# Kernel tuning notes

Measured on AMD Instinct MI355X. Metric: run time of the kernel, lower is better.

Reference implementation:

```python
import jax, jax.numpy as jnp
import numpy as np

B=4; L=1024; NF=64; DM=256; DS=16; SCS=8; NL=4; DI=512; DTR=16; DC=4; NFM=6; NH=4; SCALES=(5,20,50)

def _ln(x,g,b):
    m=x.mean(-1,keepdims=True); v=((x-m)**2).mean(-1,keepdims=True)
    return (x-m)*jax.lax.rsqrt(v+1e-5)*g+b

def _scan(dA,dBu,C):
    # sequential selective scan: h_t = dA_t*h + dBu_t ; y_t = sum_n h_t * C_t
    def step(h,inp):
        a,bu,c=inp
        h=a*h+bu
        return h, jnp.einsum('bdn,bn->bd',h,c)
    h0=jnp.zeros(dA.shape[:1]+dA.shape[2:],dA.dtype)
    _,ys=jax.lax.scan(step,h0,(dA.swapaxes(0,1),dBu.swapaxes(0,1),C.swapaxes(0,1)))
    return ys.swapaxes(0,1)  # [B,L,DI]

def _mamba(x,g,b,inw,cw,cb,xpw,dtw,dtb,Alog,Dp,outw,ds):
    # MambaBlock: LN -> SelectiveSSM -> residual (dropout=identity in eval)
    xn=_ln(x,g,b)
    u,z=jnp.split(xn@inw.T,2,-1)
    k=cw.T[:,None,:]  # torch depthwise Conv1d weight [DI,1,DC] -> WIO [DC,1,DI]
    u=jax.lax.conv_general_dilated(u,k,(1,),[(cw.shape[1]-1,0)],dimension_numbers=('NWC','WIO','NWC'),feature_group_count=u.shape[-1])+cb
    u=jax.nn.silu(u)
    A=-jnp.exp(Alog)                     # [DI,ds]
    xd=u@xpw.T                           # [B,L,DTR+2*ds]
    dt=jax.nn.softplus(xd[...,:DTR]@dtw.T+dtb)   # [B,L,DI]
    Bm=xd[...,DTR:DTR+ds]; Cm=xd[...,DTR+ds:]
    dA=jnp.exp(dt[...,None]*A)                   # [B,L,DI,ds]
    dBu=dt[...,None]*Bm[:,:,None,:]*u[...,None]  # [B,L,DI,ds]
    y=_scan(dA,dBu,Cm)+u*Dp
    return x+(y*jax.nn.silu(z))@outw.T

def _mha(x,wqkv,bqkv,wout,bout):
    Bq,S,E=x.shape; hd=E//NH
    q,k,v=jnp.split(x@wqkv.T+bqkv,3,-1)
    sp=lambda t: t.reshape(Bq,S,NH,hd).transpose(0,2,1,3)
    att=jax.nn.softmax(jnp.einsum('bhqd,bhkd->bhqk',sp(q),sp(k))*(1.0/np.sqrt(hd)),-1)
    o=jnp.einsum('bhqk,bhkd->bhqd',att,sp(v)).transpose(0,2,1,3).reshape(Bq,S,E)
    return o@wout.T+bout

def _forward(x,in_w,in_b,in_ln_g,in_ln_b,mb_ln_g,mb_ln_b,mb_in_w,mb_conv_w,mb_conv_b,mb_xp_w,mb_dt_w,mb_dt_b,mb_Alog,mb_D,mb_out_w,sc_ln_g,sc_ln_b,sc_in_w,sc_conv_w,sc_conv_b,sc_xp_w,sc_dt_w,sc_dt_b,sc_Alog,sc_D,sc_out_w,fus_qkv_w,fus_qkv_b,fus_out_w,fus_out_b,ms_out_w,ms_out_b,sa_ln1_g,sa_ln1_b,sa_ln2_g,sa_ln2_b,sa_qkv_w,sa_qkv_b,sa_out_w,sa_out_b,sa_ff1_w,sa_ff1_b,sa_ff2_w,sa_ff2_b,ev1_w,ev1_b,ev2_w,ev2_b,ttf1_w,ttf1_b,ttf2_w,ttf2_b,emb_w,emb_b):
    gelu=lambda t: jax.nn.gelu(t,approximate=False)
    h=gelu(_ln(x@in_w.T+in_b,in_ln_g,in_ln_b))
    for i in range(NL):
        h=_mamba(h,mb_ln_g[i],mb_ln_b[i],mb_in_w[i],mb_conv_w[i],mb_conv_b[i],mb_xp_w[i],mb_dt_w[i],mb_dt_b[i],mb_Alog[i],mb_D[i],mb_out_w[i],DS)
    pooled=[]
    for i,s in enumerate(SCALES):
        p=_mamba(h[:,-s:,:],sc_ln_g[i],sc_ln_b[i],sc_in_w[i],sc_conv_w[i],sc_conv_b[i],sc_xp_w[i],sc_dt_w[i],sc_dt_b[i],sc_Alog[i],sc_D[i],sc_out_w[i],SCS)
        pooled.append(p.mean(1))  # AdaptiveAvgPool1d(1)
    stack=jnp.stack(pooled,1)  # [B,3,DM]
    fused=_mha(stack,fus_qkv_w,fus_qkv_b,fus_out_w,fus_out_b).reshape(x.shape[0],-1)@ms_out_w.T+ms_out_b
    s2=stack+_mha(_ln(stack,sa_ln1_g,sa_ln1_b),sa_qkv_w,sa_qkv_b,sa_out_w,sa_out_b)
    att=s2+(gelu(_ln(s2,sa_ln2_g,sa_ln2_b)@sa_ff1_w.T+sa_ff1_b)@sa_ff2_w.T+sa_ff2_b)
    final=fused+att.mean(1)
    ev=jax.nn.softplus(gelu(final@ev1_w.T+ev1_b)@ev2_w.T+ev2_b)
    alpha=ev+1.0
    Ssum=alpha.sum(-1,keepdims=True)
    probs=alpha/Ssum; unc=(NFM+1)/Ssum
    ttf=gelu(final@ttf1_w.T+ttf1_b)@ttf2_w.T+ttf2_b
    tm=jax.nn.softplus(ttf[:,:NFM]); ts=jnp.exp(0.5*ttf[:,NFM:])
    emb=final@emb_w.T+emb_b
    # concat of (probs, evidence, alpha, uncertainty, ttf_mean, ttf_std, embedding) -> [B,162]
    return jnp.concatenate([probs,ev,alpha,unc,tm,ts,emb],-1)

def setup_inputs():
    ks=iter(jax.random.split(jax.random.key(0),64))
    nk=lambda: next(ks)
    w=lambda *s: jax.random.normal(nk(),s,jnp.float32)*0.02
    z=lambda *s: jnp.zeros(s,jnp.float32)
    o=lambda *s: jnp.ones(s,jnp.float32)
    Al=lambda n,ds: jnp.broadcast_to(jnp.log(jnp.arange(1,ds+1,dtype=jnp.float32)),(n,DI,ds))
    return dict(x=jax.random.normal(nk(),(B,L,NF),jnp.float32),
        in_w=w(DM,NF), in_b=z(DM), in_ln_g=o(DM), in_ln_b=z(DM),
        mb_ln_g=o(NL,DM), mb_ln_b=z(NL,DM), mb_in_w=w(NL,2*DI,DM), mb_conv_w=w(NL,DI,DC), mb_conv_b=z(NL,DI),
        mb_xp_w=w(NL,DTR+2*DS,DI), mb_dt_w=w(NL,DI,DTR), mb_dt_b=z(NL,DI), mb_Alog=Al(NL,DS), mb_D=o(NL,DI), mb_out_w=w(NL,DM,DI),
        sc_ln_g=o(3,DM), sc_ln_b=z(3,DM), sc_in_w=w(3,2*DI,DM), sc_conv_w=w(3,DI,DC), sc_conv_b=z(3,DI),
        sc_xp_w=w(3,DTR+2*SCS,DI), sc_dt_w=w(3,DI,DTR), sc_dt_b=z(3,DI), sc_Alog=Al(3,SCS), sc_D=o(3,DI), sc_out_w=w(3,DM,DI),
        fus_qkv_w=w(3*DM,DM), fus_qkv_b=z(3*DM), fus_out_w=w(DM,DM), fus_out_b=z(DM), ms_out_w=w(DM,3*DM), ms_out_b=z(DM),
        sa_ln1_g=o(DM), sa_ln1_b=z(DM), sa_ln2_g=o(DM), sa_ln2_b=z(DM),
        sa_qkv_w=w(3*DM,DM), sa_qkv_b=z(3*DM), sa_out_w=w(DM,DM), sa_out_b=z(DM),
        sa_ff1_w=w(4*DM,DM), sa_ff1_b=z(4*DM), sa_ff2_w=w(DM,4*DM), sa_ff2_b=z(DM),
        ev1_w=w(DM,DM), ev1_b=z(DM), ev2_w=w(NFM+1,DM), ev2_b=z(NFM+1),
        ttf1_w=w(DM//2,DM), ttf1_b=z(DM//2), ttf2_w=w(2*NFM,DM//2), ttf2_b=z(2*NFM),
        emb_w=w(DM//2,DM), emb_b=z(DM//2))

def reference(x,in_w,in_b,in_ln_g,in_ln_b,mb_ln_g,mb_ln_b,mb_in_w,mb_conv_w,mb_conv_b,mb_xp_w,mb_dt_w,mb_dt_b,mb_Alog,mb_D,mb_out_w,sc_ln_g,sc_ln_b,sc_in_w,sc_conv_w,sc_conv_b,sc_xp_w,sc_dt_w,sc_dt_b,sc_Alog,sc_D,sc_out_w,fus_qkv_w,fus_qkv_b,fus_out_w,fus_out_b,ms_out_w,ms_out_b,sa_ln1_g,sa_ln1_b,sa_ln2_g,sa_ln2_b,sa_qkv_w,sa_qkv_b,sa_out_w,sa_out_b,sa_ff1_w,sa_ff1_b,sa_ff2_w,sa_ff2_b,ev1_w,ev1_b,ev2_w,ev2_b,ttf1_w,ttf1_b,ttf2_w,ttf2_b,emb_w,emb_b):
    return _forward(x,in_w,in_b,in_ln_g,in_ln_b,mb_ln_g,mb_ln_b,mb_in_w,mb_conv_w,mb_conv_b,mb_xp_w,mb_dt_w,mb_dt_b,mb_Alog,mb_D,mb_out_w,sc_ln_g,sc_ln_b,sc_in_w,sc_conv_w,sc_conv_b,sc_xp_w,sc_dt_w,sc_dt_b,sc_Alog,sc_D,sc_out_w,fus_qkv_w,fus_qkv_b,fus_out_w,fus_out_b,ms_out_w,ms_out_b,sa_ln1_g,sa_ln1_b,sa_ln2_g,sa_ln2_b,sa_qkv_w,sa_qkv_b,sa_out_w,sa_out_b,sa_ff1_w,sa_ff1_b,sa_ff2_w,sa_ff2_b,ev1_w,ev1_b,ev2_w,ev2_b,ttf1_w,ttf1_b,ttf2_w,ttf2_b,emb_w,emb_b)
```

## Files before the change

kernel.cpp:

```cpp
#include <hip/hip_runtime.h>
#include <math.h>


typedef short short8v __attribute__((ext_vector_type(8)));
typedef float f32x4   __attribute__((ext_vector_type(4)));

__device__ __forceinline__ float geluf(float x){ return 0.5f*x*(1.0f + erff(x*0.70710678118654752f)); }
__device__ __forceinline__ float softplusf_(float x){ return (x > 20.f) ? x : log1pf(expf(x)); }
__device__ __forceinline__ unsigned short f2bf(float f){
  unsigned int u = __float_as_uint(f);
  unsigned int r = (u + 0x7FFFu + ((u >> 16) & 1u)) >> 16;
  return (unsigned short)r;
}

__device__ __forceinline__ void sc_region(int r, int& z, int& roff, int& s){
  if (r < 64){ z=0; roff=0; s=5; }
  else if (r < 192){ z=1; roff=64; s=20; }
  else { z=2; roff=192; s=50; }
}

__global__ __launch_bounds__(256) void k_f2b_all(
    const float* s0, unsigned short* d0,
    const float* s1, unsigned short* d1,
    const float* s2, unsigned short* d2,
    const float* s3, unsigned short* d3,
    const float* s4, unsigned short* d4,
    const float* s5, unsigned short* d5)
{
  int blk = blockIdx.x;
  const float* s; unsigned short* d; int base;
  if      (blk < 1024){ s=s0; d=d0; base=0; }
  else if (blk < 1536){ s=s1; d=d1; base=1024; }
  else if (blk < 1632){ s=s2; d=d2; base=1536; }
  else if (blk < 2400){ s=s3; d=d3; base=1632; }
  else if (blk < 2784){ s=s4; d=d4; base=2400; }
  else                { s=s5; d=d5; base=2784; }
  int i = ((blk - base)*256 + threadIdx.x)*4;
  float4 v = *(const float4*)(s + i);
  *(ushort4*)(d + i) = make_ushort4(f2bf(v.x), f2bf(v.y), f2bf(v.z), f2bf(v.w));
}

__global__ __launch_bounds__(256) void k_inproj(
    const float* __restrict__ x, const float* __restrict__ w,
    const float* __restrict__ b, const float* __restrict__ g,
    const float* __restrict__ beta, float* __restrict__ h)
{
  __shared__ float xr[64];
  __shared__ float r1[4], r2[4];
  int row = blockIdx.x;
  int tid = threadIdx.x;
  if (tid < 64) xr[tid] = x[row*64 + tid];
  __syncthreads();
  float acc = b[tid];
  const float* wr = w + tid*64;
  #pragma unroll
  for (int k = 0; k < 64; k++) acc += xr[k]*wr[k];
  float s1 = acc, s2 = acc*acc;
  #pragma unroll
  for (int o = 32; o > 0; o >>= 1){ s1 += __shfl_down(s1,o,64); s2 += __shfl_down(s2,o,64); }
  if ((tid & 63) == 0){ r1[tid>>6] = s1; r2[tid>>6] = s2; }
  __syncthreads();
  float S1 = r1[0]+r1[1]+r1[2]+r1[3];
  float S2 = r2[0]+r2[1]+r2[2]+r2[3];
  float m = S1*(1.f/256.f);
  float var = S2*(1.f/256.f) - m*m;
  float xn = (acc - m)*rsqrtf(var + 1e-5f)*g[tid] + beta[tid];
  h[row*256 + tid] = geluf(xn);
}

__global__ __launch_bounds__(256) void k_ln(
    const float* __restrict__ src, const float* __restrict__ g, const float* __restrict__ beta,
    unsigned short* __restrict__ dst)
{
  __shared__ float r1[4], r2[4];
  int r = blockIdx.x, tid = threadIdx.x;
  float v = src[r*256 + tid];
  float s1 = v, s2 = v*v;
  #pragma unroll
  for (int o = 32; o > 0; o >>= 1){ s1 += __shfl_down(s1,o,64); s2 += __shfl_down(s2,o,64); }
  if ((tid & 63) == 0){ r1[tid>>6] = s1; r2[tid>>6] = s2; }
  __syncthreads();
  float S1 = r1[0]+r1[1]+r1[2]+r1[3];
  float S2 = r2[0]+r2[1]+r2[2]+r2[3];
  float m = S1*(1.f/256.f);
  float var = S2*(1.f/256.f) - m*m;
  dst[r*256 + tid] = f2bf((v - m)*rsqrtf(var + 1e-5f)*g[tid] + beta[tid]);
}

__global__ __launch_bounds__(256) void k_ln_sc(
    const float* __restrict__ h, const float* __restrict__ gb, const float* __restrict__ bb,
    unsigned short* __restrict__ dst, float* __restrict__ stack)
{
  __shared__ float r1[4], r2[4];
  int r = blockIdx.x, tid = threadIdx.x;
  if (r >= 448){
    int idx = (r - 448)*256 + tid;
    if (idx < 3072) stack[idx] = 0.f;
    return;
  }
  int z, roff, s; sc_region(r, z, roff, s);
  int local = r - roff;
  if (local >= 4*s) return;
  int b = local / s, t = local % s;
  float v = h[(b*1024 + (1024 - s) + t)*256 + tid];
  const float* g = gb + z*256; const float* be = bb + z*256;
  float s1 = v, s2 = v*v;
  #pragma unroll
  for (int o = 32; o > 0; o >>= 1){ s1 += __shfl_down(s1,o,64); s2 += __shfl_down(s2,o,64); }
  if ((tid & 63) == 0){ r1[tid>>6] = s1; r2[tid>>6] = s2; }
  __syncthreads();
  float S1 = r1[0]+r1[1]+r1[2]+r1[3];
  float S2 = r2[0]+r2[1]+r2[2]+r2[3];
  float m = S1*(1.f/256.f);
  float var = S2*(1.f/256.f) - m*m;
  dst[r*256 + tid] = f2bf((v - m)*rsqrtf(var + 1e-5f)*g[tid] + be[tid]);
}

template<int MODE, int SCB>
__global__ __launch_bounds__(256) void k_mm64(
    const unsigned short* __restrict__ A, const unsigned short* __restrict__ Wb,
    float* __restrict__ C,
    const float* __restrict__ resid,
    float* __restrict__ pool_out,
    int M, int N, int K, int wstr)
{
  int tid = threadIdx.x;
  int wave = tid >> 6, lane = tid & 63;
  int mh = wave & 1, nh = wave >> 1;
  int m0 = blockIdx.y*64 + mh*32;
  int n0 = blockIdx.x*64 + nh*32;
  int z = 0, roff = 0, sc = 0;
  const unsigned short* W = Wb;
  if (SCB){ sc_region(blockIdx.y*64, z, roff, sc); W += z*wstr; }
  int lrow = lane & 15, kc = lane >> 4;
  f32x4 acc[2][2] = {{{0.f,0.f,0.f,0.f},{0.f,0.f,0.f,0.f}},{{0.f,0.f,0.f,0.f},{0.f,0.f,0.f,0.f}}};
  for (int k0 = 0; k0 < K; k0 += 32){
    short8v a[2], b[2];
    #pragma unroll
    for (int mi = 0; mi < 2; mi++){
      int r = m0 + mi*16 + lrow; r = min(r, M-1);
      a[mi] = *(const short8v*)(A + r*K + k0 + kc*8);
    }
    #pragma unroll
    for (int ni = 0; ni < 2; ni++){
      int c = n0 + ni*16 + lrow;
      b[ni] = *(const short8v*)(W + c*K + k0 + kc*8);
    }
    #pragma unroll
    for (int mi = 0; mi < 2; mi++)
      #pragma unroll
      for (int ni = 0; ni < 2; ni++)
        acc[mi][ni] = __builtin_amdgcn_mfma_f32_16x16x32_bf16(a[mi], b[ni], acc[mi][ni], 0, 0, 0);
  }
  int rb = kc*4;
  #pragma unroll
  for (int mi = 0; mi < 2; mi++){
    #pragma unroll
    for (int rr = 0; rr < 4; rr++){
      int grow = m0 + mi*16 + rb + rr;
      if (grow >= M) continue;
      #pragma unroll
      for (int ni = 0; ni < 2; ni++){
        int gcol = n0 + ni*16 + lrow;
        float v = acc[mi][ni][rr];
        if (MODE == 0){
          C[grow*N + gcol] = v;
        } else if (MODE == 1){
          C[grow*N + gcol] = resid[grow*256 + gcol] + v;
        } else {
          int local = grow - roff;
          if (local < 4*sc){
            int bb2 = local / sc, t = local % sc;
            float rv = resid[(bb2*1024 + (1024 - sc) + t)*256 + gcol] + v;
            atomicAdd(&pool_out[bb2*768 + z*256 + gcol], rv*(1.f/(float)sc));
          }
        }
      }
    }
  }
}

__global__ __launch_bounds__(256) void k_conv(
    const float* __restrict__ uz, const float* __restrict__ cw, const float* __restrict__ cb,
    float* __restrict__ uc, unsigned short* __restrict__ ucb)
{
  int row = blockIdx.x;
  int t = row & 1023;
  int tid = threadIdx.x;
  for (int d = tid; d < 512; d += 256){
    float acc = cb[d];
    const float* w = cw + d*4;
    #pragma unroll
    for (int k = 0; k < 4; k++){
      int ts = t - 3 + k;
      if (ts >= 0) acc += uz[(long)(row - (3-k))*1024 + d]*w[k];
    }
    float s = acc/(1.f + expf(-acc));
    uc[(long)row*512 + d] = s;
    ucb[(long)row*512 + d] = f2bf(s);
  }
}

__global__ __launch_bounds__(256) void k_conv_sc(
    const float* __restrict__ uz, const float* __restrict__ cwb, const float* __restrict__ cbb,
    float* __restrict__ uc, unsigned short* __restrict__ ucb)
{
  int row = blockIdx.x;
  int z, roff, s; sc_region(row, z, roff, s);
  int local = row - roff;
  if (local >= 4*s) return;
  int t = local % s;
  const float* cw = cwb + z*2048;
  const float* cb = cbb + z*512;
  int tid = threadIdx.x;
  for (int d = tid; d < 512; d += 256){
    float acc = cb[d];
    const float* w = cw + d*4;
    #pragma unroll
    for (int k = 0; k < 4; k++){
      int ts = t - 3 + k;
      if (ts >= 0) acc += uz[(long)(row - (3-k))*1024 + d]*w[k];
    }
    float sv = acc/(1.f + expf(-acc));
    uc[(long)row*512 + d] = sv;
    ucb[(long)row*512 + d] = f2bf(sv);
  }
}

template<int NT, int SCB>
__global__ __launch_bounds__(512) void k_xpdt(
    const unsigned short* __restrict__ A, const unsigned short* __restrict__ Wb,
    float* __restrict__ xdout,
    const float* __restrict__ dtwb, const float* __restrict__ dtbb,
    float* __restrict__ dtout, int M)
{
  const int K = 512;
  const int NC = NT*16;
  __shared__ float pacc[8][16][NC];
  __shared__ float sxd[16][16];
  int tid = threadIdx.x;
  int wave = tid >> 6, lane = tid & 63;
  int bm0 = blockIdx.x*16;
  const unsigned short* W = Wb;
  const float* dtw = dtwb;
  const float* dtb = dtbb;
  if (SCB){
    int z, roff, s; sc_region(bm0, z, roff, s);
    W += z*(NC*K); dtw += z*8192; dtb += z*512;
  }
  int lrow = lane & 15, kc = lane >> 4;
  int kbase = wave*64;
  f32x4 acc[NT];
  #pragma unroll
  for (int ni = 0; ni < NT; ni++) acc[ni] = (f32x4){0.f,0.f,0.f,0.f};
  #pragma unroll
  for (int k0 = 0; k0 < 64; k0 += 32){
    short8v a = *(const short8v*)(A + (long)(bm0 + lrow)*K + kbase + k0 + kc*8);
    #pragma unroll
    for (int ni = 0; ni < NT; ni++){
      short8v b = *(const short8v*)(W + (ni*16 + lrow)*K + kbase + k0 + kc*8);
      acc[ni] = __builtin_amdgcn_mfma_f32_16x16x32_bf16(a, b, acc[ni], 0, 0, 0);
    }
  }
  int rb = kc*4;
  #pragma unroll
  for (int rr = 0; rr < 4; rr++)
    #pragma unroll
    for (int ni = 0; ni < NT; ni++)
      pacc[wave][rb + rr][ni*16 + lrow] = acc[ni][rr];
  __syncthreads();
  for (int e = tid; e < 16*NC; e += 512){
    int r = e / NC, c = e % NC;
    float v = pacc[0][r][c] + pacc[1][r][c] + pacc[2][r][c] + pacc[3][r][c]
            + pacc[4][r][c] + pacc[5][r][c] + pacc[6][r][c] + pacc[7][r][c];
    xdout[(bm0 + r)*NC + c] = v;
    if (c < 16) sxd[r][c] = v;
  }
  __syncthreads();
  int d0 = tid;
  float w0[16];
  #pragma unroll
  for (int j = 0; j < 16; j++) w0[j] = dtw[d0*16 + j];
  float b0 = dtb[d0];
  #pragma unroll
  for (int r = 0; r < 16; r++){
    float a0 = b0;
    #pragma unroll
    for (int j = 0; j < 16; j++)
      a0 = fmaf(sxd[r][j], w0[j], a0);
    dtout[(bm0 + r)*512 + d0] = softplusf_(a0);
  }
}

__global__ __launch_bounds__(256) void k_scan_p1y(
    const float* __restrict__ dt, const float* __restrict__ uc,
    const float* __restrict__ xd, const float* __restrict__ Alog,
    float* __restrict__ hend, float* __restrict__ sdtb,
    float* __restrict__ yloc, float* __restrict__ Scum)
{
  const int CL = 64, NCH = 16;
  __shared__ float sdt[64][64], suc[64][64];
  __shared__ float sBC[64][32];
  int tid = threadIdx.x;
  int dblk = blockIdx.x;
  int b = blockIdx.y, ch = blockIdx.z;
  int t0 = ch*CL;
  for (int e = tid; e < CL*16; e += 256){
    int t = e >> 4, q = (e & 15)*4;
    long off = (long)(b*1024 + t0 + t)*512 + dblk*64 + q;
    *(float4*)&sdt[t][q] = *(const float4*)(dt + off);
    *(float4*)&suc[t][q] = *(const float4*)(uc + off);
  }
  for (int e = tid; e < CL*8; e += 256){
    int t = e >> 3, q = (e & 7)*4;
    *(float4*)&sBC[t][q] = *(const float4*)(xd + (long)(b*1024 + t0 + t)*48 + 16 + q);
  }
  __syncthreads();
  if (tid < 64){
    int d = dblk*64 + tid;
    float A[16];
    #pragma unroll
    for (int n = 0; n < 16; n++) A[n] = -__expf(Alog[d*16 + n]);
    float h[16];
    #pragma unroll
    for (int n = 0; n < 16; n++) h[n] = 0.f;
    float Ss = 0.f;
    #pragma unroll 2
    for (int t = 0; t < CL; t++){
      float dtv = sdt[t][tid];
      float uv  = suc[t][tid];
      Ss += dtv;
      float du = dtv*uv;
      float y = 0.f;
      #pragma unroll
      for (int n = 0; n < 16; n++){
        h[n] = fmaf(__expf(dtv*A[n]), h[n], du*sBC[t][n]);
        y = fmaf(h[n], sBC[t][16+n], y);
      }
      long row = (long)(b*1024 + t0 + t);
      yloc[row*512 + d] = y;
      Scum[row*512 + d] = Ss;
    }
    int base = ((b*NCH + ch)*512 + d)*16;
    #pragma unroll
    for (int q = 0; q < 4; q++)
      *(float4*)(hend + base + q*4) = make_float4(h[q*4], h[q*4+1], h[q*4+2], h[q*4+3]);
    sdtb[(b*NCH + ch)*512 + d] = Ss;
  }
}

__global__ __launch_bounds__(256) void k_scomb(
    const float* __restrict__ hend, const float* __restrict__ sdtb,
    const float* __restrict__ Alog, float* __restrict__ hstart,
    float* __restrict__ Aneg)
{
  const int NCH = 16;
  int idx = blockIdx.x*256 + threadIdx.x;
  int low = idx & 8191;
  int d = (idx >> 4) & 511, b = idx >> 13;
  float A = -__expf(Alog[low]);
  if (b == 0) Aneg[low] = A;
  float hs = 0.f;
  hstart[(b*NCH)*8192 + low] = 0.f;
  for (int c = 0; c < NCH-1; c++){
    float S  = sdtb[(b*NCH + c)*512 + d];
    float he = hend[(b*NCH + c)*8192 + low];
    hs = fmaf(__expf(A*S), hs, he);
    hstart[(b*NCH + c + 1)*8192 + low] = hs;
  }
}

__global__ __launch_bounds__(256) void k_corr(
    const float* __restrict__ yloc, const float* __restrict__ Scum,
    const float* __restrict__ hstart, const float* __restrict__ Aneg,
    const float* __restrict__ xd, const float* __restrict__ uc,
    const float* __restrict__ uz, const float* __restrict__ Dp,
    unsigned short* __restrict__ yg)
{
  __shared__ float sC[16];
  int row = blockIdx.x, tid = threadIdx.x;
  int b = row >> 10, t = row & 1023, ch = t >> 6;
  if (tid < 16) sC[tid] = xd[row*48 + 32 + tid];
  __syncthreads();
  #pragma unroll
  for (int rep = 0; rep < 2; rep++){
    int d = tid + rep*256;
    float Ss = Scum[row*512 + d];
    float y  = yloc[row*512 + d];
    const float* hs = hstart + ((b*16 + ch)*512 + d)*16;
    const float* An = Aneg + d*16;
    #pragma unroll
    for (int n = 0; n < 16; n++)
      y = fmaf(__expf(An[n]*Ss)*hs[n], sC[n], y);
    float uv = uc[row*512 + d];
    y = fmaf(uv, Dp[d], y);
    float zv = uz[(long)row*1024 + 512 + d];
    yg[row*512 + d] = f2bf(y*(zv/(1.f + __expf(-zv))));
  }
}

__global__ __launch_bounds__(64) void k_scan_sc(
    const float* __restrict__ dt, const float* __restrict__ uc,
    const float* __restrict__ uz, const float* __restrict__ xd,
    const float* __restrict__ Alogb, const float* __restrict__ Dpb,
    unsigned short* __restrict__ yg)
{
  __shared__ float sdt[52][64], suc[52][64], sz[52][64];
  __shared__ float sBC[52][16];
  int tid = threadIdx.x;
  int dblk = blockIdx.x;
  int d = dblk*64 + tid;
  int b = blockIdx.y, z = blockIdx.z;
  int s = (z==0) ? 5 : (z==1) ? 20 : 50;
  int roff = (z==0) ? 0 : (z==1) ? 64 : 192;
  const float* Alog = Alogb + z*4096;
  const float* Dp   = Dpb + z*512;
  float A[8];
  #pragma unroll
  for (int n = 0; n < 8; n++) A[n] = -__expf(Alog[d*8 + n]);
  float Dv = Dp[d];
  for (int e = tid; e < s*16; e += 64){
    int t = e >> 4, q = (e & 15)*4;
    long row = (long)(roff + b*s + t);
    *(float4*)&sdt[t][q] = *(const float4*)(dt + row*512 + dblk*64 + q);
    *(float4*)&suc[t][q] = *(const float4*)(uc + row*512 + dblk*64 + q);
    *(float4*)&sz[t][q]  = *(const float4*)(uz + row*1024 + 512 + dblk*64 + q);
  }
  for (int e = tid; e < s*4; e += 64){
    int t = e >> 2, q = (e & 3)*4;
    long row = (long)(roff + b*s + t);
    *(float4*)&sBC[t][q] = *(const float4*)(xd + row*32 + 16 + q);
  }
  __syncthreads();
  float h[8];
  #pragma unroll
  for (int n = 0; n < 8; n++) h[n] = 0.f;
  for (int t = 0; t < s; t++){
    float dtv = sdt[t][tid];
    float uv  = suc[t][tid];
    float zv  = sz[t][tid];
    float du = dtv*uv;
    float y = 0.f;
    #pragma unroll
    for (int n = 0; n < 8; n++){
      h[n] = fmaf(__expf(dtv*A[n]), h[n], du*sBC[t][n]);
      y = fmaf(h[n], sBC[t][8+n], y);
    }
    y = fmaf(uv, Dv, y);
    float gate = zv/(1.f + __expf(-zv));
    yg[(long)(roff + b*s + t)*512 + d] = f2bf(y*gate);
  }
}

template<int M, int ACT, int RES>
__global__ __launch_bounds__(256) void k_tw(
    const float* __restrict__ A, const float* __restrict__ W,
    const float* __restrict__ bias, float* __restrict__ out,
    const float* __restrict__ resid, int N, int K, int ostride, int ocoff)
{
  extern __shared__ float sx[];
  int tid = threadIdx.x;
  for (int e = tid*4; e < M*K; e += 1024)
    *(float4*)&sx[e] = *(const float4*)(A + e);
  __syncthreads();
  int wave = tid >> 6, lane = tid & 63;
  int c = blockIdx.x*4 + wave;
  if (c >= N) return;
  float acc[M];
  #pragma unroll
  for (int r = 0; r < M; r++) acc[r] = 0.f;
  for (int k = lane*4; k < K; k += 256){
    float4 w4 = *(const float4*)(W + c*K + k);
    #pragma unroll
    for (int r = 0; r < M; r++){
      float4 x4 = *(float4*)&sx[r*K + k];
      acc[r] = fmaf(x4.x,w4.x,fmaf(x4.y,w4.y,fmaf(x4.z,w4.z,fmaf(x4.w,w4.w,acc[r]))));
    }
  }
  #pragma unroll
  for (int r = 0; r < M; r++){
    #pragma unroll
    for (int o = 32; o > 0; o >>= 1) acc[r] += __shfl_down(acc[r], o, 64);
  }
  if (lane == 0){
    float bv = bias[c];
    #pragma unroll
    for (int r = 0; r < M; r++){
      float v = acc[r] + bv;
      if (ACT == 1) v = geluf(v);
      if (RES == 1) v += resid[r*256 + c];
      out[r*ostride + ocoff + c] = v;
    }
  }
}

__global__ __launch_bounds__(256) void k_t_ln(
    const float* __restrict__ src, const float* __restrict__ g, const float* __restrict__ b,
    float* __restrict__ dst)
{
  __shared__ float r1[4], r2[4];
  int r = blockIdx.x, tid = threadIdx.x;
  float v = src[r*256 + tid];
  float s1 = v, s2 = v*v;
  #pragma unroll
  for (int o = 32; o > 0; o >>= 1){ s1 += __shfl_down(s1,o,64); s2 += __shfl_down(s2,o,64); }
  if ((tid & 63) == 0){ r1[tid>>6] = s1; r2[tid>>6] = s2; }
  __syncthreads();
  float S1 = r1[0]+r1[1]+r1[2]+r1[3];
  float S2 = r2[0]+r2[1]+r2[2]+r2[3];
  float m = S1*(1.f/256.f);
  float var = S2*(1.f/256.f) - m*m;
  dst[r*256 + tid] = (v - m)*rsqrtf(var + 1e-5f)*g[tid] + b[tid];
}

__global__ __launch_bounds__(256) void k_t_att(
    const float* __restrict__ qkv, float* __restrict__ ov)
{
  __shared__ float att[36];
  int b = blockIdx.x, tid = threadIdx.x;
  if (tid < 36){
    int hh = tid/9, r = (tid%9)/3, c = tid%3;
    float s = 0.f;
    const float* qp = qkv + (b*3 + r)*768 + hh*64;
    const float* kp = qkv + (b*3 + c)*768 + 256 + hh*64;
    for (int k = 0; k < 64; k++) s += qp[k]*kp[k];
    att[hh*9 + r*3 + c] = s*0.125f;
  }
  __syncthreads();
  if (tid < 12){
    int hh = tid/3, r = tid%3;
    float a0 = att[hh*9+r*3+0], a1 = att[hh*9+r*3+1], a2 = att[hh*9+r*3+2];
    float m = fmaxf(a0, fmaxf(a1, a2));
    float e0 = expf(a0-m), e1 = expf(a1-m), e2 = expf(a2-m);
    float s = e0+e1+e2;
    att[hh*9+r*3+0] = e0/s; att[hh*9+r*3+1] = e1/s; att[hh*9+r*3+2] = e2/s;
  }
  __syncthreads();
  for (int e = tid; e < 768; e += 256){
    int p = e >> 8, i = e & 255, hh = i >> 6;
    ov[(b*3 + p)*256 + i] = att[hh*9+p*3+0]*qkv[(b*3+0)*768+512+i]
                          + att[hh*9+p*3+1]*qkv[(b*3+1)*768+512+i]
                          + att[hh*9+p*3+2]*qkv[(b*3+2)*768+512+i];
  }
}

__global__ __launch_bounds__(256) void k_t_final(
    const float* __restrict__ fusedv, const float* __restrict__ s2f, float* __restrict__ finalv)
{
  int b = blockIdx.x, c = threadIdx.x;
  finalv[b*256 + c] = fusedv[b*256 + c] +
    (s2f[(b*3+0)*256 + c] + s2f[(b*3+1)*256 + c] + s2f[(b*3+2)*256 + c])*(1.f/3.f);
}

__global__ __launch_bounds__(64) void k_t_fin(
    const float* __restrict__ evraw, const float* __restrict__ ttraw, float* __restrict__ out)
{
  __shared__ float ev[7];
  __shared__ float S;
  int b = blockIdx.x, tid = threadIdx.x;
  if (tid < 7) ev[tid] = softplusf_(evraw[b*7 + tid]);
  __syncthreads();
  if (tid == 0){
    float s = 0.f;
    for (int j = 0; j < 7; j++) s += ev[j] + 1.f;
    S = s;
  }
  __syncthreads();
  float* ob = out + b*162;
  if (tid < 7){
    float al = ev[tid] + 1.f;
    ob[tid] = al / S;
    ob[7 + tid] = ev[tid];
    ob[14 + tid] = al;
  }
  if (tid == 0) ob[21] = 7.f / S;
  if (tid < 6){
    ob[22 + tid] = softplusf_(ttraw[b*12 + tid]);
    ob[28 + tid] = expf(0.5f*ttraw[b*12 + 6 + tid]);
  }
}

extern "C" void kernel_launch(void* const* d_in, const int* in_sizes, int n_in,
                              void* d_out, int out_size, void* d_ws, size_t ws_size,
                              hipStream_t stream)
{
  const float* x         = (const float*)d_in[0];
  const float* in_w      = (const float*)d_in[1];
  const float* in_b      = (const float*)d_in[2];
  const float* in_ln_g   = (const float*)d_in[3];
  const float* in_ln_b   = (const float*)d_in[4];
  const float* mb_ln_g   = (const float*)d_in[5];
  const float* mb_ln_b   = (const float*)d_in[6];
  const float* mb_in_w   = (const float*)d_in[7];
  const float* mb_conv_w = (const float*)d_in[8];
  const float* mb_conv_b = (const float*)d_in[9];
  const float* mb_xp_w   = (const float*)d_in[10];
  const float* mb_dt_w   = (const float*)d_in[11];
  const float* mb_dt_b   = (const float*)d_in[12];
  const float* mb_Alog   = (const float*)d_in[13];
  const float* mb_D      = (const float*)d_in[14];
  const float* mb_out_w  = (const float*)d_in[15];
  const float* sc_ln_g   = (const float*)d_in[16];
  const float* sc_ln_b   = (const float*)d_in[17];
  const float* sc_in_w   = (const float*)d_in[18];
  const float* sc_conv_w = (const float*)d_in[19];
  const float* sc_conv_b = (const float*)d_in[20];
  const float* sc_xp_w   = (const float*)d_in[21];
  const float* sc_dt_w   = (const float*)d_in[22];
  const float* sc_dt_b   = (const float*)d_in[23];
  const float* sc_Alog   = (const float*)d_in[24];
  const float* sc_D      = (const float*)d_in[25];
  const float* sc_out_w  = (const float*)d_in[26];
  const float* fus_qkv_w = (const float*)d_in[27];
  const float* fus_qkv_b = (const float*)d_in[28];
  const float* fus_out_w = (const float*)d_in[29];
  const float* fus_out_b = (const float*)d_in[30];
  const float* ms_out_w  = (const float*)d_in[31];
  const float* ms_out_b  = (const float*)d_in[32];
  const float* sa_ln1_g  = (const float*)d_in[33];
  const float* sa_ln1_b  = (const float*)d_in[34];
  const float* sa_ln2_g  = (const float*)d_in[35];
  const float* sa_ln2_b  = (const float*)d_in[36];
  const float* sa_qkv_w  = (const float*)d_in[37];
  const float* sa_qkv_b  = (const float*)d_in[38];
  const float* sa_out_w  = (const float*)d_in[39];
  const float* sa_out_b  = (const float*)d_in[40];
  const float* sa_ff1_w  = (const float*)d_in[41];
  const float* sa_ff1_b  = (const float*)d_in[42];
  const float* sa_ff2_w  = (const float*)d_in[43];
  const float* sa_ff2_b  = (const float*)d_in[44];
  const float* ev1_w     = (const float*)d_in[45];
  const float* ev1_b     = (const float*)d_in[46];
  const float* ev2_w     = (const float*)d_in[47];
  const float* ev2_b     = (const float*)d_in[48];
  const float* ttf1_w    = (const float*)d_in[49];
  const float* ttf1_b    = (const float*)d_in[50];
  const float* ttf2_w    = (const float*)d_in[51];
  const float* ttf2_b    = (const float*)d_in[52];
  const float* emb_w     = (const float*)d_in[53];
  const float* emb_b     = (const float*)d_in[54];

  float* ws = (float*)d_ws;
  float* h     = ws;
  float* uz    = h    + 1048576;
  float* uc    = uz   + 4194304;
  float* dtb_  = uc   + 2097152;
  float* xd    = dtb_ + 2097152;
  float* stack = xd   + 196608;
  float* hend   = stack + 4096;
  float* hstart = hend + 524288;
  float* sdtb   = hstart + 524288;
  float* yloc   = sdtb + 32768;
  float* Scum   = yloc + 2097152;
  float* Aneg   = Scum + 2097152;
  float* qkvF   = Aneg + 8192;
  float* ovF    = qkvF + 9216;
  float* moF    = ovF  + 3072;
  float* fusedv = moF  + 3072;
  float* lnbuf  = fusedv + 1024;
  float* qkvS   = lnbuf + 3072;
  float* ovS    = qkvS + 9216;
  float* s2     = ovS  + 3072;
  float* ln2r   = s2   + 3072;
  float* hid    = ln2r + 3072;
  float* s2f    = hid  + 12288;
  float* finalv = s2f  + 3072;
  float* evh    = finalv + 1024;
  float* tth    = evh  + 1024;
  float* evraw  = tth  + 512;
  float* ttraw  = evraw + 32;
  float* fp32_end = ttraw + 64;
  unsigned short* bfb = (unsigned short*)fp32_end;
  unsigned short* xnb    = bfb;
  unsigned short* ucb    = xnb + 1048576;
  unsigned short* ygb    = ucb + 2097152;
  unsigned short* wmbin  = ygb + 2097152;
  unsigned short* wmbout = wmbin + 1048576;
  unsigned short* wmbxp  = wmbout + 524288;
  unsigned short* wscin  = wmbxp + 98304;
  unsigned short* wscout = wscin + 786432;
  unsigned short* wscxp  = wscout + 393216;

  k_f2b_all<<<2832, 256, 0, stream>>>(mb_in_w, wmbin, mb_out_w, wmbout, mb_xp_w, wmbxp,
                                      sc_in_w, wscin, sc_out_w, wscout, sc_xp_w, wscxp);

  k_inproj<<<4096, 256, 0, stream>>>(x, in_w, in_b, in_ln_g, in_ln_b, h);

  for (int l = 0; l < 4; l++){
    const float* Al = mb_Alog + l*8192;
    k_ln<<<4096, 256, 0, stream>>>(h, mb_ln_g + l*256, mb_ln_b + l*256, xnb);
    {
      dim3 g(16, 64);
      k_mm64<0,0><<<g, 256, 0, stream>>>(xnb, wmbin + l*262144, uz,
                                         nullptr, nullptr, 4096, 1024, 256, 0);
    }
    k_conv<<<4096, 256, 0, stream>>>(uz, mb_conv_w + l*2048, mb_conv_b + l*512, uc, ucb);
    k_xpdt<3,0><<<256, 512, 0, stream>>>(ucb, wmbxp + l*24576, xd,
                                         mb_dt_w + l*8192, mb_dt_b + l*512, dtb_, 4096);
    {
      dim3 g(8, 4, 16);
      k_scan_p1y<<<g, 256, 0, stream>>>(dtb_, uc, xd, Al, hend, sdtb, yloc, Scum);
      k_scomb<<<128, 256, 0, stream>>>(hend, sdtb, Al, hstart, Aneg);
      k_corr<<<4096, 256, 0, stream>>>(yloc, Scum, hstart, Aneg, xd, uc, uz,
                                       mb_D + l*512, ygb);
    }
    {
      dim3 g(4, 64);
      k_mm64<1,0><<<g, 256, 0, stream>>>(ygb, wmbout + l*131072, h,
                                         h, nullptr, 4096, 256, 512, 0);
    }
  }

  k_ln_sc<<<460, 256, 0, stream>>>(h, sc_ln_g, sc_ln_b, xnb, stack);
  {
    dim3 g(16, 7);
    k_mm64<0,1><<<g, 256, 0, stream>>>(xnb, wscin, uz, nullptr, nullptr,
                                       448, 1024, 256, 262144);
  }
  k_conv_sc<<<448, 256, 0, stream>>>(uz, sc_conv_w, sc_conv_b, uc, ucb);
  k_xpdt<2,1><<<28, 512, 0, stream>>>(ucb, wscxp, xd, sc_dt_w, sc_dt_b, dtb_, 448);
  {
    dim3 g(8, 4, 3);
    k_scan_sc<<<g, 64, 0, stream>>>(dtb_, uc, uz, xd, sc_Alog, sc_D, ygb);
  }
  {
    dim3 g(4, 7);
    k_mm64<2,1><<<g, 256, 0, stream>>>(ygb, wscout, nullptr, h, stack,
                                       448, 256, 512, 131072);
  }

  float* dout = (float*)d_out;
  k_tw<12,0,0><<<192, 256, 12*256*4, stream>>>(stack, fus_qkv_w, fus_qkv_b, qkvF, nullptr, 768, 256, 768, 0);
  k_t_att<<<4, 256, 0, stream>>>(qkvF, ovF);
  k_tw<12,0,0><<<64, 256, 12*256*4, stream>>>(ovF, fus_out_w, fus_out_b, moF, nullptr, 256, 256, 256, 0);
  k_tw<4,0,0><<<64, 256, 4*768*4, stream>>>(moF, ms_out_w, ms_out_b, fusedv, nullptr, 256, 768, 256, 0);
  k_t_ln<<<12, 256, 0, stream>>>(stack, sa_ln1_g, sa_ln1_b, lnbuf);
  k_tw<12,0,0><<<192, 256, 12*256*4, stream>>>(lnbuf, sa_qkv_w, sa_qkv_b, qkvS, nullptr, 768, 256, 768, 0);
  k_t_att<<<4, 256, 0, stream>>>(qkvS, ovS);
  k_tw<12,0,1><<<64, 256, 12*256*4, stream>>>(ovS, sa_out_w, sa_out_b, s2, stack, 256, 256, 256, 0);
  k_t_ln<<<12, 256, 0, stream>>>(s2, sa_ln2_g, sa_ln2_b, ln2r);
  k_tw<12,1,0><<<256, 256, 12*256*4, stream>>>(ln2r, sa_ff1_w, sa_ff1_b, hid, nullptr, 1024, 256, 1024, 0);
  k_tw<12,0,1><<<64, 256, 12*1024*4, stream>>>(hid, sa_ff2_w, sa_ff2_b, s2f, s2, 256, 1024, 256, 0);
  k_t_final<<<4, 256, 0, stream>>>(fusedv, s2f, finalv);
  k_tw<4,1,0><<<64, 256, 4*256*4, stream>>>(finalv, ev1_w, ev1_b, evh, nullptr, 256, 256, 256, 0);
  k_tw<4,0,0><<<2, 256, 4*256*4, stream>>>(evh, ev2_w, ev2_b, evraw, nullptr, 7, 256, 7, 0);
  k_tw<4,1,0><<<32, 256, 4*256*4, stream>>>(finalv, ttf1_w, ttf1_b, tth, nullptr, 128, 256, 128, 0);
  k_tw<4,0,0><<<3, 256, 4*128*4, stream>>>(tth, ttf2_w, ttf2_b, ttraw, nullptr, 12, 128, 12, 0);
  k_tw<4,0,0><<<32, 256, 4*256*4, stream>>>(finalv, emb_w, emb_b, dout, nullptr, 128, 256, 162, 34);
  k_t_fin<<<4, 64, 0, stream>>>(evraw, ttraw, dout);
}
```

Measured before the change: 624.1 us.

## Store gate and conv output as bf16 and batch small tail kernels

The in-projection GEMM now writes the u half as fp32 into a narrower buffer and the z gate half as bf16. The fp32 conv output is dropped, so the scan and correction kernels read bf16 u and z and convert them on load. Separately, the tail launches are merged: the two QKV projections, both attentions, both output projections and the three head projections each run as one combined kernel. This cuts memory traffic and launch count, at the cost of bf16 rounding on u and z inside the scan.

New measurement: 620.7 us. No clear change (-0.5%).

```diff
diff --git a/kernel.cpp b/kernel.cpp
--- a/kernel.cpp
+++ b/kernel.cpp
@@ -11,6 +11,9 @@
   unsigned int u = __float_as_uint(f);
   unsigned int r = (u + 0x7FFFu + ((u >> 16) & 1u)) >> 16;
   return (unsigned short)r;
+}
+__device__ __forceinline__ float bf2f(unsigned short u){
+  return __uint_as_float(((unsigned int)u) << 16);
 }
 
 __device__ __forceinline__ void sc_region(int r, int& z, int& roff, int& s){
@@ -122,6 +125,7 @@
     float* __restrict__ C,
     const float* __restrict__ resid,
     float* __restrict__ pool_out,
+    unsigned short* __restrict__ zgb,
     int M, int N, int K, int wstr)
 {
   int tid = threadIdx.x;
@@ -164,7 +168,8 @@
         int gcol = n0 + ni*16 + lrow;
         float v = acc[mi][ni][rr];
         if (MODE == 0){
-          C[grow*N + gcol] = v;
+          if (gcol < 512) C[(long)grow*512 + gcol] = v;
+          else zgb[(long)grow*512 + (gcol - 512)] = f2bf(v);
         } else if (MODE == 1){
           C[grow*N + gcol] = resid[grow*256 + gcol] + v;
         } else {
@@ -181,8 +186,8 @@
 }
 
 __global__ __launch_bounds__(256) void k_conv(
-    const float* __restrict__ uz, const float* __restrict__ cw, const float* __restrict__ cb,
-    float* __restrict__ uc, unsigned short* __restrict__ ucb)
+    const float* __restrict__ uu, const float* __restrict__ cw, const float* __restrict__ cb,
+    unsigned short* __restrict__ ucb)
 {
   int row = blockIdx.x;
   int t = row & 1023;
@@ -193,17 +198,16 @@
     #pragma unroll
     for (int k = 0; k < 4; k++){
       int ts = t - 3 + k;
-      if (ts >= 0) acc += uz[(long)(row - (3-k))*1024 + d]*w[k];
+      if (ts >= 0) acc += uu[(long)(row - (3-k))*512 + d]*w[k];
     }
     float s = acc/(1.f + expf(-acc));
-    uc[(long)row*512 + d] = s;
     ucb[(long)row*512 + d] = f2bf(s);
   }
 }
 
 __global__ __launch_bounds__(256) void k_conv_sc(
-    const float* __restrict__ uz, const float* __restrict__ cwb, const float* __restrict__ cbb,
-    float* __restrict__ uc, unsigned short* __restrict__ ucb)
+    const float* __restrict__ uu, const float* __restrict__ cwb, const float* __restrict__ cbb,
+    unsigned short* __restrict__ ucb)
 {
   int row = blockIdx.x;
   int z, roff, s; sc_region(row, z, roff, s);
@@ -219,10 +223,9 @@
     #pragma unroll
     for (int k = 0; k < 4; k++){
       int ts = t - 3 + k;
-      if (ts >= 0) acc += uz[(long)(row - (3-k))*1024 + d]*w[k];
+      if (ts >= 0) acc += uu[(long)(row - (3-k))*512 + d]*w[k];
     }
     float sv = acc/(1.f + expf(-acc));
-    uc[(long)row*512 + d] = sv;
     ucb[(long)row*512 + d] = f2bf(sv);
   }
 }
@@ -293,7 +296,7 @@
 }
 
 __global__ __launch_bounds__(256) void k_scan_p1y(
-    const float* __restrict__ dt, const float* __restrict__ uc,
+    const float* __restrict__ dt, const unsigned short* __restrict__ ucb,
     const float* __restrict__ xd, const float* __restrict__ Alog,
     float* __restrict__ hend, float* __restrict__ sdtb,
     float* __restrict__ yloc, float* __restrict__ Scum)
@@ -309,7 +312,13 @@
     int t = e >> 4, q = (e & 15)*4;
     long off = (long)(b*1024 + t0 + t)*512 + dblk*64 + q;
     *(float4*)&sdt[t][q] = *(const float4*)(dt + off);
-    *(float4*)&suc[t][q] = *(const float4*)(uc + off);
+  }
+  for (int e = tid; e < CL*8; e += 256){
+    int t = e >> 3, q = (e & 7)*8;
+    long off = (long)(b*1024 + t0 + t)*512 + dblk*64 + q;
+    short8v u8 = *(const short8v*)(ucb + off);
+    #pragma unroll
+    for (int j = 0; j < 8; j++) suc[t][q + j] = bf2f((unsigned short)u8[j]);
   }
   for (int e = tid; e < CL*8; e += 256){
     int t = e >> 3, q = (e & 7)*4;
@@ -373,8 +382,8 @@
 __global__ __launch_bounds__(256) void k_corr(
     const float* __restrict__ yloc, const float* __restrict__ Scum,
     const float* __restrict__ hstart, const float* __restrict__ Aneg,
-    const float* __restrict__ xd, const float* __restrict__ uc,
-    const float* __restrict__ uz, const float* __restrict__ Dp,
+    const float* __restrict__ xd, const unsigned short* __restrict__ ucb,
+    const unsigned short* __restrict__ zgb, const float* __restrict__ Dp,
     unsigned short* __restrict__ yg)
 {
   __shared__ float sC[16];
@@ -392,16 +401,16 @@
     #pragma unroll
     for (int n = 0; n < 16; n++)
       y = fmaf(__expf(An[n]*Ss)*hs[n], sC[n], y);
-    float uv = uc[row*512 + d];
+    float uv = bf2f(ucb[(long)row*512 + d]);
     y = fmaf(uv, Dp[d], y);
-    float zv = uz[(long)row*1024 + 512 + d];
+    float zv = bf2f(zgb[(long)row*512 + d]);
     yg[row*512 + d] = f2bf(y*(zv/(1.f + __expf(-zv))));
   }
 }
 
 __global__ __launch_bounds__(64) void k_scan_sc(
-    const float* __restrict__ dt, const float* __restrict__ uc,
-    const float* __restrict__ uz, const float* __restrict__ xd,
+    const float* __restrict__ dt, const unsigned short* __restrict__ ucb,
+    const unsigned short* __restrict__ zgb, const float* __restrict__ xd,
     const float* __restrict__ Alogb, const float* __restrict__ Dpb,
     unsigned short* __restrict__ yg)
 {
@@ -423,8 +432,17 @@
     int t = e >> 4, q = (e & 15)*4;
     long row = (long)(roff + b*s + t);
     *(float4*)&sdt[t][q] = *(const float4*)(dt + row*512 + dblk*64 + q);
-    *(float4*)&suc[t][q] = *(const float4*)(uc + row*512 + dblk*64 + q);
-    *(float4*)&sz[t][q]  = *(const float4*)(uz + row*1024 + 512 + dblk*64 + q);
+  }
+  for (int e = tid; e < s*8; e += 64){
+    int t = e >> 3, q = (e & 7)*8;
+    long row = (long)(roff + b*s + t);
+    short8v u8 = *(const short8v*)(ucb + row*512 + dblk*64 + q);
+    short8v z8 = *(const short8v*)(zgb + row*512 + dblk*64 + q);
+    #pragma unroll
+    for (int j = 0; j < 8; j++){
+      suc[t][q + j] = bf2f((unsigned short)u8[j]);
+      sz[t][q + j]  = bf2f((unsigned short)z8[j]);
+    }
   }
   for (int e = tid; e < s*4; e += 64){
     int t = e >> 2, q = (e & 3)*4;
@@ -494,30 +512,56 @@
   }
 }
 
-__global__ __launch_bounds__(256) void k_t_ln(
-    const float* __restrict__ src, const float* __restrict__ g, const float* __restrict__ b,
-    float* __restrict__ dst)
-{
-  __shared__ float r1[4], r2[4];
-  int r = blockIdx.x, tid = threadIdx.x;
-  float v = src[r*256 + tid];
-  float s1 = v, s2 = v*v;
-  #pragma unroll
-  for (int o = 32; o > 0; o >>= 1){ s1 += __shfl_down(s1,o,64); s2 += __shfl_down(s2,o,64); }
-  if ((tid & 63) == 0){ r1[tid>>6] = s1; r2[tid>>6] = s2; }
-  __syncthreads();
-  float S1 = r1[0]+r1[1]+r1[2]+r1[3];
-  float S2 = r2[0]+r2[1]+r2[2]+r2[3];
-  float m = S1*(1.f/256.f);
-  float var = S2*(1.f/256.f) - m*m;
-  dst[r*256 + tid] = (v - m)*rsqrtf(var + 1e-5f)*g[tid] + b[tid];
-}
-
-__global__ __launch_bounds__(256) void k_t_att(
-    const float* __restrict__ qkv, float* __restrict__ ov)
+__global__ __launch_bounds__(256) void k_qkv2(
+    const float* __restrict__ A0, const float* __restrict__ A1,
+    const float* __restrict__ W0, const float* __restrict__ B0,
+    const float* __restrict__ W1, const float* __restrict__ B1,
+    float* __restrict__ O0, float* __restrict__ O1)
+{
+  __shared__ float sx[3072];
+  int tid = threadIdx.x;
+  int sel = blockIdx.x >= 192;
+  const float* A = sel ? A1 : A0;
+  for (int e = tid*4; e < 3072; e += 1024)
+    *(float4*)&sx[e] = *(const float4*)(A + e);
+  __syncthreads();
+  int wave = tid >> 6, lane = tid & 63;
+  int c = (blockIdx.x - (sel ? 192 : 0))*4 + wave;
+  const float* W = sel ? W1 : W0;
+  const float* B = sel ? B1 : B0;
+  float* O = sel ? O1 : O0;
+  float acc[12];
+  #pragma unroll
+  for (int r = 0; r < 12; r++) acc[r] = 0.f;
+  {
+    int k = lane*4;
+    float4 w4 = *(const float4*)(W + c*256 + k);
+    #pragma unroll
+    for (int r = 0; r < 12; r++){
+      float4 x4 = *(float4*)&sx[r*256 + k];
+      acc[r] = fmaf(x4.x,w4.x,fmaf(x4.y,w4.y,fmaf(x4.z,w4.z,fmaf(x4.w,w4.w,acc[r]))));
+    }
+  }
+  #pragma unroll
+  for (int r = 0; r < 12; r++){
+    #pragma unroll
+    for (int o = 32; o > 0; o >>= 1) acc[r] += __shfl_down(acc[r], o, 64);
+  }
+  if (lane == 0){
+    float bv = B[c];
+    #pragma unroll
+    for (int r = 0; r < 12; r++) O[r*768 + c] = acc[r] + bv;
+  }
+}
+
+__global__ __launch_bounds__(256) void k_att2(
+    const float* __restrict__ qkvF, float* __restrict__ ovF,
+    const float* __restrict__ qkvS, float* __restrict__ ovS)
 {
   __shared__ float att[36];
-  int b = blockIdx.x, tid = threadIdx.x;
+  int sel = blockIdx.x >> 2, b = blockIdx.x & 3, tid = threadIdx.x;
+  const float* qkv = sel ? qkvS : qkvF;
+  float* ov = sel ? ovS : ovF;
   if (tid < 36){
     int hh = tid/9, r = (tid%9)/3, c = tid%3;
     float s = 0.f;
@@ -542,6 +586,116 @@
                           + att[hh*9+p*3+1]*qkv[(b*3+1)*768+512+i]
                           + att[hh*9+p*3+2]*qkv[(b*3+2)*768+512+i];
   }
+}
+
+__global__ __launch_bounds__(256) void k_out2(
+    const float* __restrict__ ovF, const float* __restrict__ ovS,
+    const float* __restrict__ fow, const float* __restrict__ fob,
+    const float* __restrict__ sow, const float* __restrict__ sob,
+    const float* __restrict__ stack, float* __restrict__ moF, float* __restrict__ s2)
+{
+  __shared__ float sx[3072];
+  int tid = threadIdx.x;
+  int sel = blockIdx.x >= 64;
+  const float* A = sel ? ovS : ovF;
+  for (int e = tid*4; e < 3072; e += 1024)
+    *(float4*)&sx[e] = *(const float4*)(A + e);
+  __syncthreads();
+  int wave = tid >> 6, lane = tid & 63;
+  int c = (blockIdx.x - (sel ? 64 : 0))*4 + wave;
+  const float* W = sel ? sow : fow;
+  const float* B = sel ? sob : fob;
+  float acc[12];
+  #pragma unroll
+  for (int r = 0; r < 12; r++) acc[r] = 0.f;
+  {
+    int k = lane*4;
+    float4 w4 = *(const float4*)(W + c*256 + k);
+    #pragma unroll
+    for (int r = 0; r < 12; r++){
+      float4 x4 = *(float4*)&sx[r*256 + k];
+      acc[r] = fmaf(x4.x,w4.x,fmaf(x4.y,w4.y,fmaf(x4.z,w4.z,fmaf(x4.w,w4.w,acc[r]))));
+    }
+  }
+  #pragma unroll
+  for (int r = 0; r < 12; r++){
+    #pragma unroll
+    for (int o = 32; o > 0; o >>= 1) acc[r] += __shfl_down(acc[r], o, 64);
+  }
+  if (lane == 0){
+    float bv = B[c];
+    #pragma unroll
+    for (int r = 0; r < 12; r++){
+      float v = acc[r] + bv;
+      if (sel) s2[r*256 + c] = v + stack[r*256 + c];
+      else     moF[r*256 + c] = v;
+    }
+  }
+}
+
+__global__ __launch_bounds__(256) void k_heads(
+    const float* __restrict__ finalv,
+    const float* __restrict__ e1w, const float* __restrict__ e1b, float* __restrict__ evh,
+    const float* __restrict__ t1w, const float* __restrict__ t1b, float* __restrict__ tth,
+    const float* __restrict__ ew, const float* __restrict__ eb, float* __restrict__ dout)
+{
+  __shared__ float sx[1024];
+  int tid = threadIdx.x;
+  if (tid < 256){
+    float4 v = *(const float4*)(finalv + tid*4);
+    *(float4*)&sx[tid*4] = v;
+  }
+  __syncthreads();
+  int wave = tid >> 6, lane = tid & 63;
+  int blk = blockIdx.x;
+  const float* W; const float* B; int c; int which;
+  if (blk < 64){ which = 0; c = blk*4 + wave; W = e1w; B = e1b; }
+  else if (blk < 96){ which = 1; c = (blk - 64)*4 + wave; W = t1w; B = t1b; }
+  else { which = 2; c = (blk - 96)*4 + wave; W = ew; B = eb; }
+  float acc[4] = {0.f,0.f,0.f,0.f};
+  {
+    int k = lane*4;
+    float4 w4 = *(const float4*)(W + c*256 + k);
+    #pragma unroll
+    for (int r = 0; r < 4; r++){
+      float4 x4 = *(float4*)&sx[r*256 + k];
+      acc[r] = fmaf(x4.x,w4.x,fmaf(x4.y,w4.y,fmaf(x4.z,w4.z,fmaf(x4.w,w4.w,acc[r]))));
+    }
+  }
+  #pragma unroll
+  for (int r = 0; r < 4; r++){
+    #pragma unroll
+    for (int o = 32; o > 0; o >>= 1) acc[r] += __shfl_down(acc[r], o, 64);
+  }
+  if (lane == 0){
+    float bv = B[c];
+    #pragma unroll
+    for (int r = 0; r < 4; r++){
+      float v = acc[r] + bv;
+      if (which == 0) evh[r*256 + c] = geluf(v);
+      else if (which == 1) tth[r*128 + c] = geluf(v);
+      else dout[r*162 + 34 + c] = v;
+    }
+  }
+}
+
+__global__ __launch_bounds__(256) void k_t_ln(
+    const float* __restrict__ src, const float* __restrict__ g, const float* __restrict__ b,
+    float* __restrict__ dst)
+{
+  __shared__ float r1[4], r2[4];
+  int r = blockIdx.x, tid = threadIdx.x;
+  float v = src[r*256 + tid];
+  float s1 = v, s2 = v*v;
+  #pragma unroll
+  for (int o = 32; o > 0; o >>= 1){ s1 += __shfl_down(s1,o,64); s2 += __shfl_down(s2,o,64); }
+  if ((tid & 63) == 0){ r1[tid>>6] = s1; r2[tid>>6] = s2; }
+  __syncthreads();
+  float S1 = r1[0]+r1[1]+r1[2]+r1[3];
+  float S2 = r2[0]+r2[1]+r2[2]+r2[3];
+  float m = S1*(1.f/256.f);
+  float var = S2*(1.f/256.f) - m*m;
+  dst[r*256 + tid] = (v - m)*rsqrtf(var + 1e-5f)*g[tid] + b[tid];
 }
 
 __global__ __launch_bounds__(256) void k_t_final(
@@ -642,9 +796,8 @@
 
   float* ws = (float*)d_ws;
   float* h     = ws;
-  float* uz    = h    + 1048576;
-  float* uc    = uz   + 4194304;
-  float* dtb_  = uc   + 2097152;
+  float* uu    = h    + 1048576;
+  float* dtb_  = uu   + 2097152;
   float* xd    = dtb_ + 2097152;
   float* stack = xd   + 196608;
   float* hend   = stack + 4096;
@@ -673,7 +826,8 @@
   unsigned short* bfb = (unsigned short*)fp32_end;
   unsigned short* xnb    = bfb;
   unsigned short* ucb    = xnb + 1048576;
-  unsigned short* ygb    = ucb + 2097152;
+  unsigned short* zgb    = ucb + 2097152;
+  unsigned short* ygb    = zgb + 2097152;
   unsigned short* wmbin  = ygb + 2097152;
   unsigned short* wmbout = wmbin + 1048576;
   unsigned short* wmbxp  = wmbout + 524288;
@@ -691,61 +845,59 @@
     k_ln<<<4096, 256, 0, stream>>>(h, mb_ln_g + l*256, mb_ln_b + l*256, xnb);
     {
       dim3 g(16, 64);
-      k_mm64<0,0><<<g, 256, 0, stream>>>(xnb, wmbin + l*262144, uz,
-                                         nullptr, nullptr, 4096, 1024, 256, 0);
-    }
-    k_conv<<<4096, 256, 0, stream>>>(uz, mb_conv_w + l*2048, mb_conv_b + l*512, uc, ucb);
+      k_mm64<0,0><<<g, 256, 0, stream>>>(xnb, wmbin + l*262144, uu,
+                                         nullptr, nullptr, zgb, 4096, 1024, 256, 0);
+    }
+    k_conv<<<4096, 256, 0, stream>>>(uu, mb_conv_w + l*2048, mb_conv_b + l*512, ucb);
     k_xpdt<3,0><<<256, 512, 0, stream>>>(ucb, wmbxp + l*24576, xd,
                                          mb_dt_w + l*8192, mb_dt_b + l*512, dtb_, 4096);
     {
       dim3 g(8, 4, 16);
-      k_scan_p1y<<<g, 256, 0, stream>>>(dtb_, uc, xd, Al, hend, sdtb, yloc, Scum);
+      k_scan_p1y<<<g, 256, 0, stream>>>(dtb_, ucb, xd, Al, hend, sdtb, yloc, Scum);
       k_scomb<<<128, 256, 0, stream>>>(hend, sdtb, Al, hstart, Aneg);
-      k_corr<<<4096, 256, 0, stream>>>(yloc, Scum, hstart, Aneg, xd, uc, uz,
+      k_corr<<<4096, 256, 0, stream>>>(yloc, Scum, hstart, Aneg, xd, ucb, zgb,
                                        mb_D + l*512, ygb);
     }
     {
       dim3 g(4, 64);
       k_mm64<1,0><<<g, 256, 0, stream>>>(ygb, wmbout + l*131072, h,
-                                         h, nullptr, 4096, 256, 512, 0);
+                                         h, nullptr, nullptr, 4096, 256, 512, 0);
     }
   }
 
   k_ln_sc<<<460, 256, 0, stream>>>(h, sc_ln_g, sc_ln_b, xnb, stack);
   {
     dim3 g(16, 7);
-    k_mm64<0,1><<<g, 256, 0, stream>>>(xnb, wscin, uz, nullptr, nullptr,
+    k_mm64<0,1><<<g, 256, 0, stream>>>(xnb, wscin, uu, nullptr, nullptr, zgb,
                                        448, 1024, 256, 262144);
   }
-  k_conv_sc<<<448, 256, 0, stream>>>(uz, sc_conv_w, sc_conv_b, uc, ucb);
+  k_conv_sc<<<448, 256, 0, stream>>>(uu, sc_conv_w, sc_conv_b, ucb);
   k_xpdt<2,1><<<28, 512, 0, stream>>>(ucb, wscxp, xd, sc_dt_w, sc_dt_b, dtb_, 448);
   {
     dim3 g(8, 4, 3);
-    k_scan_sc<<<g, 64, 0, stream>>>(dtb_, uc, uz, xd, sc_Alog, sc_D, ygb);
+    k_scan_sc<<<g, 64, 0, stream>>>(dtb_, ucb, zgb, xd, sc_Alog, sc_D, ygb);
   }
   {
     dim3 g(4, 7);
-    k_mm64<2,1><<<g, 256, 0, stream>>>(ygb, wscout, nullptr, h, stack,
+    k_mm64<2,1><<<g, 256, 0, stream>>>(ygb, wscout, nullptr, h, stack, nullptr,
                                        448, 256, 512, 131072);
   }
 
   float* dout = (float*)d_out;
-  k_tw<12,0,0><<<192, 256, 12*256*4, stream>>>(stack, fus_qkv_w, fus_qkv_b, qkvF, nullptr, 768, 256, 768, 0);
-  k_t_att<<<4, 256, 0, stream>>>(qkvF, ovF);
-  k_tw<12,0,0><<<64, 256, 12*256*4, stream>>>(ovF, fus_out_w, fus_out_b, moF, nullptr, 256, 256, 256, 0);
+  k_t_ln<<<12, 256, 0, stream>>>(stack, sa_ln1_g, sa_ln1_b, lnbuf);
+  k_qkv2<<<384, 256, 0, stream>>>(stack, lnbuf, fus_qkv_w, fus_qkv_b,
+                                  sa_qkv_w, sa_qkv_b, qkvF, qkvS);
+  k_att2<<<8, 256, 0, stream>>>(qkvF, ovF, qkvS, ovS);
+  k_out2<<<128, 256, 0, stream>>>(ovF, ovS, fus_out_w, fus_out_b,
+                                  sa_out_w, sa_out_b, stack, moF, s2);
   k_tw<4,0,0><<<64, 256, 4*768*4, stream>>>(moF, ms_out_w, ms_out_b, fusedv, nullptr, 256, 768, 256, 0);
-  k_t_ln<<<12, 256, 0, stream>>>(stack, sa_ln1_g, sa_ln1_b, lnbuf);
-  k_tw<12,0,0><<<192, 256, 12*256*4, stream>>>(lnbuf, sa_qkv_w, sa_qkv_b, qkvS, nullptr, 768, 256, 768, 0);
-  k_t_att<<<4, 256, 0, stream>>>(qkvS, ovS);
-  k_tw<12,0,1><<<64, 256, 12*256*4, stream>>>(ovS, sa_out_w, sa_out_b, s2, stack, 256, 256, 256, 0);
   k_t_ln<<<12, 256, 0, stream>>>(s2, sa_ln2_g, sa_ln2_b, ln2r);
   k_tw<12,1,0><<<256, 256, 12*256*4, stream>>>(ln2r, sa_ff1_w, sa_ff1_b, hid, nullptr, 1024, 256, 1024, 0);
   k_tw<12,0,1><<<64, 256, 12*1024*4, stream>>>(hid, sa_ff2_w, sa_ff2_b, s2f, s2, 256, 1024, 256, 0);
   k_t_final<<<4, 256, 0, stream>>>(fusedv, s2f, finalv);
-  k_tw<4,1,0><<<64, 256, 4*256*4, stream>>>(finalv, ev1_w, ev1_b, evh, nullptr, 256, 256, 256, 0);
+  k_heads<<<128, 256, 0, stream>>>(finalv, ev1_w, ev1_b, evh, ttf1_w, ttf1_b, tth,
+                                   emb_w, emb_b, dout);
   k_tw<4,0,0><<<2, 256, 4*256*4, stream>>>(evh, ev2_w, ev2_b, evraw, nullptr, 7, 256, 7, 0);
-  k_tw<4,1,0><<<32, 256, 4*256*4, stream>>>(finalv, ttf1_w, ttf1_b, tth, nullptr, 128, 256, 128, 0);
   k_tw<4,0,0><<<3, 256, 4*128*4, stream>>>(tth, ttf2_w, ttf2_b, ttraw, nullptr, 12, 128, 12, 0);
-  k_tw<4,0,0><<<32, 256, 4*256*4, stream>>>(finalv, emb_w, emb_b, dout, nullptr, 128, 256, 162, 34);
   k_t_fin<<<4, 64, 0, stream>>>(evraw, ttraw, dout);
 }
```
